# Kernel tuning notes

Measured on AMD Instinct MI355X. Metric: run time of the kernel, lower is better.

## Reference

```python
import jax, jax.numpy as jnp
import numpy as np

B, T, C, HD = 4, 4096, 1024, 64

def setup_inputs() -> dict:
    key = jax.random.key(0)
    k1, k2, k3, k4 = jax.random.split(key, 4)
    x = jax.random.normal(k1, (B, T, C), dtype=jnp.float32)
    scale = 1.0 / np.sqrt(C)
    Wq = jax.random.normal(k2, (C, HD), dtype=jnp.float32) * scale
    Wk = jax.random.normal(k3, (C, HD), dtype=jnp.float32) * scale
    Wv = jax.random.normal(k4, (C, HD), dtype=jnp.float32) * scale
    return {"x": x, "Wq": Wq, "Wk": Wk, "Wv": Wv}

def reference(x, Wq, Wk, Wv):
    # q,k,v: [B,T,HD]
    q = jnp.einsum('btc,ch->bth', x, Wq)
    k = jnp.einsum('btc,ch->bth', x, Wk)
    v = jnp.einsum('btc,ch->bth', x, Wv)
    hd = q.shape[-1]
    scores = jnp.einsum('bth,bsh->bts', q, k) / jnp.sqrt(jnp.float32(hd))  # [B,T,T]
    causal = jnp.tril(jnp.ones((scores.shape[1], scores.shape[1]), dtype=bool))
    scores = jnp.where(causal, scores, -jnp.inf)
    attn = jax.nn.softmax(scores, axis=-1)
    return jnp.einsum('bts,bsh->bth', attn, v)  # [B,T,HD]
```

## Files before the change

### kernel.cpp

```cpp
#include <hip/hip_runtime.h>
#include <hip/hip_bf16.h>

typedef __attribute__((ext_vector_type(8))) short bf16x8;
typedef __attribute__((ext_vector_type(4))) short bf16x4;
typedef __attribute__((ext_vector_type(4))) float f32x4;
typedef __attribute__((ext_vector_type(4))) int   i32x4;

#define C2LOG 0.18033688011112042f

__device__ __forceinline__ short f2bf(float f) {
    union { float f; unsigned u; } v; v.f = f;
    unsigned r = v.u + 0x7fff + ((v.u >> 16) & 1);
    return (short)(r >> 16);
}
__device__ __forceinline__ unsigned packbf(float a, float b) {
    return (unsigned)(unsigned short)f2bf(a) | ((unsigned)(unsigned short)f2bf(b) << 16);
}
__device__ __forceinline__ float bf2f(short s) {
    union { unsigned u; float f; } v; v.u = ((unsigned)(unsigned short)s) << 16;
    return v.f;
}

#define BB 4
#define TT 4096
#define CC 1024
#define HD 64
#define NTASK_PB 144
#define NTASK (BB * NTASK_PB)

__global__ void prep_w(const float* __restrict__ Wq, const float* __restrict__ Wk,
                       const float* __restrict__ Wv, short* __restrict__ Wt) {
    const int n = blockIdx.x;
    const float* W = (n < 64) ? Wq : (n < 128) ? Wk : Wv;
    const int col = n & 63;
    for (int k = threadIdx.x; k < CC; k += blockDim.x)
        Wt[n * CC + k] = f2bf(W[k * HD + col]);
}

__global__ __launch_bounds__(512) void proj_qkv(const float* __restrict__ x,
        const short* __restrict__ Wt, short* __restrict__ Q,
        short* __restrict__ K, short* __restrict__ Vt) {
    __shared__ short xs[2][32 * 72];
    __shared__ short wsm[2][192 * 64];

    const int tid  = threadIdx.x;
    const int lane = tid & 63;
    const int wv   = tid >> 6;
    const int lm   = lane & 15;
    const int lg   = lane >> 4;
    const int mhalf = wv & 1;
    const int ngrp  = wv >> 1;
    const int mbase = blockIdx.x * 32;

    const int xr  = tid >> 4;
    const int xq4 = tid & 15;
    const float* xrow = x + (size_t)(mbase + xr) * CC;

    int wsrow[3], wscol[3];
    #pragma unroll
    for (int it = 0; it < 3; ++it) {
        const int off = it * 8192 + wv * 1024 + lane * 16;
        wsrow[it] = off >> 7;
        wscol[it] = (off & 127) ^ ((wsrow[it] & 7) << 4);
    }

#define STAGE_W(bufidx, kc)                                                           \
    {                                                                                 \
        _Pragma("unroll")                                                             \
        for (int it = 0; it < 3; ++it) {                                              \
            const char* src = (const char*)(Wt + (size_t)wsrow[it] * CC + (kc) * 64)  \
                              + wscol[it];                                            \
            char* dst = (char*)&wsm[bufidx][0] + it * 8192 + wv * 1024;               \
            __builtin_amdgcn_global_load_lds(                                         \
                (const __attribute__((address_space(1))) unsigned*)src,               \
                (__attribute__((address_space(3))) unsigned*)dst, 16, 0, 0);          \
        }                                                                             \
    }

#define CONV_X(bufidx, xv)                                                            \
    {                                                                                 \
        bf16x4 bv;                                                                    \
        bv[0] = f2bf((xv).x); bv[1] = f2bf((xv).y);                                   \
        bv[2] = f2bf((xv).z); bv[3] = f2bf((xv).w);                                   \
        *reinterpret_cast<bf16x4*>(&xs[bufidx][xr * 72 + xq4 * 4]) = bv;              \
    }

    f32x4 acc[3];
    #pragma unroll
    for (int i = 0; i < 3; ++i) acc[i] = f32x4{0.f, 0.f, 0.f, 0.f};

    {
        float4 v = *reinterpret_cast<const float4*>(xrow + xq4 * 4);
        CONV_X(0, v)
        STAGE_W(0, 0)
    }
    asm volatile("s_waitcnt vmcnt(0)" ::: "memory");
    __syncthreads();

    const int arow = mhalf * 16 + lm;
    int buf = 0;
    for (int kc = 0; kc < 16; ++kc) {
        float4 nv;
        const bool more = (kc < 15);
        if (more) {
            nv = *reinterpret_cast<const float4*>(xrow + (kc + 1) * 64 + xq4 * 4);
            STAGE_W(buf ^ 1, kc + 1)
        }

        bf16x8 a0 = *reinterpret_cast<const bf16x8*>(&xs[buf][arow * 72 + lg * 8]);
        bf16x8 a1 = *reinterpret_cast<const bf16x8*>(&xs[buf][arow * 72 + 32 + lg * 8]);
        #pragma unroll
        for (int c = 0; c < 3; ++c) {
            const int brow = (ngrp * 3 + c) * 16 + lm;
            const int sw = (brow & 7) << 4;
            bf16x8 b0 = *reinterpret_cast<const bf16x8*>(
                (const char*)&wsm[buf][0] + brow * 128 + ((lg * 16) ^ sw));
            bf16x8 b1 = *reinterpret_cast<const bf16x8*>(
                (const char*)&wsm[buf][0] + brow * 128 + ((64 + lg * 16) ^ sw));
            acc[c] = __builtin_amdgcn_mfma_f32_16x16x32_bf16(a0, b0, acc[c], 0, 0, 0);
            acc[c] = __builtin_amdgcn_mfma_f32_16x16x32_bf16(a1, b1, acc[c], 0, 0, 0);
        }

        if (more) CONV_X(buf ^ 1, nv)
        asm volatile("s_waitcnt vmcnt(0)" ::: "memory");
        __syncthreads();
        buf ^= 1;
    }
#undef STAGE_W
#undef CONV_X

    const int mrow = mbase + mhalf * 16 + lg * 4;
    #pragma unroll
    for (int c = 0; c < 3; ++c) {
        const int cn = ngrp * 3 + c;
        if (cn < 4) {
            #pragma unroll
            for (int r = 0; r < 4; ++r)
                Q[(size_t)(mrow + r) * HD + cn * 16 + lm] = f2bf(acc[c][r]);
        } else if (cn < 8) {
            #pragma unroll
            for (int r = 0; r < 4; ++r)
                K[(size_t)(mrow + r) * HD + (cn - 4) * 16 + lm] = f2bf(acc[c][r]);
        } else {
            const int bb   = mbase >> 12;
            const int tloc = (mbase & 4095) + mhalf * 16 + lg * 4;
            bf16x4 v4;
            #pragma unroll
            for (int r = 0; r < 4; ++r) v4[r] = f2bf(acc[c][r]);
            *reinterpret_cast<bf16x4*>(
                Vt + (size_t)bb * (HD * TT) + (size_t)((cn - 8) * 16 + lm) * TT + tloc) = v4;
        }
    }
}

__global__ __launch_bounds__(512, 4) void attn(const short* __restrict__ Q,
        const short* __restrict__ K, const short* __restrict__ Vt,
        short* __restrict__ Opart, float* __restrict__ Mpart,
        float* __restrict__ Lpart) {
    __shared__ short ks[2][64 * 64];
    __shared__ short vs[2][64 * 64];

    const int tid  = threadIdx.x;
    const int lane = tid & 63;
    const int wv   = tid >> 6;
    const int lm   = lane & 15;
    const int lg   = lane >> 4;

    const int task = blockIdx.x;
    const int b  = task / NTASK_PB;
    int t_in = task - b * NTASK_PB;
    int g = 0;
    while (t_in >= 2 * (g + 1) * (g + 2)) ++g;
    const int idx = t_in - 2 * g * (g + 1);
    const int i   = 4 * g + idx / (g + 1);
    const int seg = idx % (g + 1);
    const int S   = g + 1;
    const int niter = 2 * i + 2;
    const int qbase = i * 128;

    const size_t qkb = (size_t)b * TT * HD;
    const size_t vtb = (size_t)b * HD * TT;
    const int qrow = qbase + wv * 16;
    const int tmax = (qrow + 15) >> 6;

    bf16x8 qf0 = *reinterpret_cast<const bf16x8*>(Q + qkb + (size_t)(qrow + lm) * HD + lg * 8);
    bf16x8 qf1 = *reinterpret_cast<const bf16x8*>(Q + qkb + (size_t)(qrow + lm) * HD + 32 + lg * 8);

    f32x4 o[4];
    #pragma unroll
    for (int c = 0; c < 4; ++c) o[c] = f32x4{0.f, 0.f, 0.f, 0.f};
    float mrun = -1e30f, lrun = 0.f;

    const int srcA = lm + ((lane & 16) << 1);
    const int srcB = srcA + 16;
    const bool hihalf = (lane & 32) != 0;

    const int lds_off = (wv << 10) + (lane << 4);
    const int srow    = lds_off >> 7;
    const int scolb   = (lds_off & 127) ^ ((srow & 7) << 4);

#define STAGE_KV(bufidx, tt)                                                          \
    {                                                                                 \
        const char* ksrc = (const char*)(K + qkb) + (tt) * 8192 + (srow << 7) + scolb;\
        char* kdst = (char*)&ks[bufidx][0] + (wv << 10);                              \
        __builtin_amdgcn_global_load_lds(                                             \
            (const __attribute__((address_space(1))) unsigned*)ksrc,                  \
            (__attribute__((address_space(3))) unsigned*)kdst, 16, 0, 0);             \
        const char* vsrc = (const char*)(Vt + vtb) + (size_t)srow * (TT * 2)          \
                           + (tt) * 128 + scolb;                                      \
        char* vdst = (char*)&vs[bufidx][0] + (wv << 10);                              \
        __builtin_amdgcn_global_load_lds(                                             \
            (const __attribute__((address_space(1))) unsigned*)vsrc,                  \
            (__attribute__((address_space(3))) unsigned*)vdst, 16, 0, 0);             \
    }

    STAGE_KV(0, seg)
    asm volatile("s_waitcnt vmcnt(0)" ::: "memory");
    __syncthreads();

    int buf = 0;
    for (int t = seg; t < niter; t += S) {
        const int tn = t + S;
        if (tn < niter) STAGE_KV(buf ^ 1, tn)

        if (t <= tmax) {
            const short* ksb = &ks[buf][0];
            const short* vsb = &vs[buf][0];
            const int kv = t * 64;

            f32x4 st[4];
            #pragma unroll
            for (int kt = 0; kt < 4; ++kt) {
                const int krow = kt * 16 + lm;
                const int sw = (krow & 7) << 4;
                bf16x8 k0 = *reinterpret_cast<const bf16x8*>(
                    (const char*)ksb + krow * 128 + ((lg * 16) ^ sw));
                bf16x8 k1 = *reinterpret_cast<const bf16x8*>(
                    (const char*)ksb + krow * 128 + ((64 + lg * 16) ^ sw));
                f32x4 a = f32x4{0.f, 0.f, 0.f, 0.f};
                a = __builtin_amdgcn_mfma_f32_16x16x32_bf16(k0, qf0, a, 0, 0, 0);
                a = __builtin_amdgcn_mfma_f32_16x16x32_bf16(k1, qf1, a, 0, 0, 0);
                st[kt] = a;
            }
            float s2[4][4];
            #pragma unroll
            for (int kt = 0; kt < 4; ++kt)
                #pragma unroll
                for (int r = 0; r < 4; ++r) s2[kt][r] = st[kt][r] * C2LOG;
            if (kv + 63 > qrow) {
                const int qg = qrow + lm;
                #pragma unroll
                for (int kt = 0; kt < 4; ++kt)
                    #pragma unroll
                    for (int r = 0; r < 4; ++r)
                        if (kv + kt * 16 + lg * 4 + r > qg) s2[kt][r] = -1e30f;
            }
            float mloc = s2[0][0];
            #pragma unroll
            for (int kt = 0; kt < 4; ++kt)
                #pragma unroll
                for (int r = 0; r < 4; ++r) mloc = fmaxf(mloc, s2[kt][r]);
            mloc = fmaxf(mloc, __shfl_xor(mloc, 16));
            mloc = fmaxf(mloc, __shfl_xor(mloc, 32));
            const float mnew = fmaxf(mrun, mloc);
            const float alpha = __builtin_amdgcn_exp2f(mrun - mnew);
            mrun = mnew;

            float p[4][4];
            float rs = 0.f;
            #pragma unroll
            for (int kt = 0; kt < 4; ++kt)
                #pragma unroll
                for (int r = 0; r < 4; ++r) {
                    p[kt][r] = __builtin_amdgcn_exp2f(s2[kt][r] - mnew);
                    rs += p[kt][r];
                }
            rs += __shfl_xor(rs, 16);
            rs += __shfl_xor(rs, 32);
            lrun = lrun * alpha + rs;

            unsigned u[4][2];
            #pragma unroll
            for (int kt = 0; kt < 4; ++kt) {
                u[kt][0] = packbf(p[kt][0], p[kt][1]);
                u[kt][1] = packbf(p[kt][2], p[kt][3]);
            }
            #pragma unroll
            for (int c = 0; c < 4; ++c)
                #pragma unroll
                for (int r = 0; r < 4; ++r) o[c][r] *= alpha;

            #pragma unroll
            for (int h = 0; h < 2; ++h) {
                const int b0 = __shfl((int)u[2 * h][0], srcA);
                const int c0 = __shfl((int)u[2 * h + 1][0], srcA);
                const int b1 = __shfl((int)u[2 * h][1], srcA);
                const int c1 = __shfl((int)u[2 * h + 1][1], srcA);
                const int b2 = __shfl((int)u[2 * h][0], srcB);
                const int c2 = __shfl((int)u[2 * h + 1][0], srcB);
                const int b3 = __shfl((int)u[2 * h][1], srcB);
                const int c3 = __shfl((int)u[2 * h + 1][1], srcB);
                union { i32x4 iv; bf16x8 v; } cv;
                cv.iv = i32x4{ hihalf ? c0 : b0, hihalf ? c1 : b1,
                               hihalf ? c2 : b2, hihalf ? c3 : b3 };
                #pragma unroll
                for (int c = 0; c < 4; ++c) {
                    const int vrow = c * 16 + lm;
                    const int sw = (vrow & 7) << 4;
                    bf16x8 va = *reinterpret_cast<const bf16x8*>(
                        (const char*)vsb + vrow * 128 + ((h * 64 + lg * 16) ^ sw));
                    o[c] = __builtin_amdgcn_mfma_f32_16x16x32_bf16(va, cv.v, o[c], 0, 0, 0);
                }
            }
        }

        asm volatile("s_waitcnt vmcnt(0)" ::: "memory");
        __syncthreads();
        buf ^= 1;
    }
#undef STAGE_KV

    short* Ob = Opart + (size_t)task * (128 * HD);
    #pragma unroll
    for (int c = 0; c < 4; ++c) {
        bf16x4 ov;
        #pragma unroll
        for (int r = 0; r < 4; ++r) ov[r] = f2bf(o[c][r]);
        *reinterpret_cast<bf16x4*>(&Ob[(wv * 16 + lm) * HD + c * 16 + lg * 4]) = ov;
    }
    if (lg == 0) {
        Mpart[task * 128 + wv * 16 + lm] = mrun;
        Lpart[task * 128 + wv * 16 + lm] = lrun;
    }
}

__global__ __launch_bounds__(256) void combine(const short* __restrict__ Opart,
        const float* __restrict__ Mpart, const float* __restrict__ Lpart,
        float* __restrict__ out) {
    const int b   = blockIdx.x >> 8;
    const int rem = blockIdx.x & 255;
    const int i   = rem >> 3;
    const int rr  = rem & 7;
    const int g = i >> 2;
    const int S = g + 1;
    const int task0 = b * NTASK_PB + 2 * g * (g + 1) + (i - 4 * g) * (g + 1);
    const int qbase = i * 128;

    const int tid = threadIdx.x;
    const int row = rr * 16 + (tid >> 4);
    const int cb  = (tid & 15) << 2;

    float mmax = -1e30f;
    float ms[8];
    for (int s = 0; s < S; ++s) {
        ms[s] = Mpart[(task0 + s) * 128 + row];
        mmax = fmaxf(mmax, ms[s]);
    }
    float lsum = 0.f;
    float a0 = 0.f, a1 = 0.f, a2 = 0.f, a3 = 0.f;
    for (int s = 0; s < S; ++s) {
        const float w = __builtin_amdgcn_exp2f(ms[s] - mmax);
        lsum += Lpart[(task0 + s) * 128 + row] * w;
        bf16x4 ov = *reinterpret_cast<const bf16x4*>(
            &Opart[((size_t)(task0 + s) * 128 + row) * HD + cb]);
        a0 += bf2f(ov[0]) * w;
        a1 += bf2f(ov[1]) * w;
        a2 += bf2f(ov[2]) * w;
        a3 += bf2f(ov[3]) * w;
    }
    const float inv = 1.0f / lsum;
    f32x4 res{ a0 * inv, a1 * inv, a2 * inv, a3 * inv };
    *reinterpret_cast<f32x4*>(
        &out[((size_t)b * TT + qbase + row) * HD + cb]) = res;
}

extern "C" void kernel_launch(void* const* d_in, const int* in_sizes, int n_in,
                              void* d_out, int out_size, void* d_ws, size_t ws_size,
                              hipStream_t stream) {
    const float* x  = (const float*)d_in[0];
    const float* Wq = (const float*)d_in[1];
    const float* Wk = (const float*)d_in[2];
    const float* Wv = (const float*)d_in[3];
    float* out = (float*)d_out;

    char* ws = (char*)d_ws;
    short* Wt    = (short*)(ws);
    short* Q     = (short*)(ws + 393216);
    short* K     = (short*)(ws + 2490368);
    short* Vt    = (short*)(ws + 4587520);
    short* Opart = (short*)(ws + 6684672);
    float* Mpart = (float*)(ws + 16121856);
    float* Lpart = (float*)(ws + 16416768);

    hipLaunchKernelGGL(prep_w,   dim3(192),   dim3(256), 0, stream, Wq, Wk, Wv, Wt);
    hipLaunchKernelGGL(proj_qkv, dim3(512),   dim3(512), 0, stream, x, Wt, Q, K, Vt);
    hipLaunchKernelGGL(attn,     dim3(NTASK), dim3(512), 0, stream, Q, K, Vt,
                       Opart, Mpart, Lpart);
    hipLaunchKernelGGL(combine,  dim3(1024),  dim3(256), 0, stream,
                       Opart, Mpart, Lpart, out);
}
```

Before: 68.34 us.

## Process 32 query rows per wave in attention to reuse K/V LDS fragments

The attention block drops from 8 to 4 waves, and each wave now handles two 16-row query tiles. Every K and V fragment read from LDS therefore feeds two MFMAs instead of one, halving LDS read traffic per FLOP. Each thread stages twice as many K/V chunks per tile. In exchange, register pressure roughly doubles (two accumulator sets and duplicated softmax state), the launch bound changes to 256 threads with min 3 blocks, and fewer waves are available to hide latency.

```diff
diff --git a/kernel.cpp b/kernel.cpp
--- a/kernel.cpp
+++ b/kernel.cpp
@@ -153,7 +153,7 @@
     }
 }
 
-__global__ __launch_bounds__(512, 4) void attn(const short* __restrict__ Q,
+__global__ __launch_bounds__(256, 3) void attn(const short* __restrict__ Q,
         const short* __restrict__ K, const short* __restrict__ Vt,
         short* __restrict__ Opart, float* __restrict__ Mpart,
         float* __restrict__ Lpart) {
@@ -176,42 +176,52 @@
     const int seg = idx % (g + 1);
     const int S   = g + 1;
     const int niter = 2 * i + 2;
-    const int qbase = i * 128;
 
     const size_t qkb = (size_t)b * TT * HD;
     const size_t vtb = (size_t)b * HD * TT;
-    const int qrow = qbase + wv * 16;
-    const int tmax = (qrow + 15) >> 6;
+    const int qrow = i * 128 + wv * 32;
+    const int tmax = (qrow + 31) >> 6;
 
     bf16x8 qf0 = *reinterpret_cast<const bf16x8*>(Q + qkb + (size_t)(qrow + lm) * HD + lg * 8);
     bf16x8 qf1 = *reinterpret_cast<const bf16x8*>(Q + qkb + (size_t)(qrow + lm) * HD + 32 + lg * 8);
-
-    f32x4 o[4];
-    #pragma unroll
-    for (int c = 0; c < 4; ++c) o[c] = f32x4{0.f, 0.f, 0.f, 0.f};
-    float mrun = -1e30f, lrun = 0.f;
+    bf16x8 qf2 = *reinterpret_cast<const bf16x8*>(Q + qkb + (size_t)(qrow + 16 + lm) * HD + lg * 8);
+    bf16x8 qf3 = *reinterpret_cast<const bf16x8*>(Q + qkb + (size_t)(qrow + 16 + lm) * HD + 32 + lg * 8);
+
+    f32x4 oA[4], oB[4];
+    #pragma unroll
+    for (int c = 0; c < 4; ++c) { oA[c] = f32x4{0.f,0.f,0.f,0.f}; oB[c] = f32x4{0.f,0.f,0.f,0.f}; }
+    float mrunA = -1e30f, lrunA = 0.f;
+    float mrunB = -1e30f, lrunB = 0.f;
 
     const int srcA = lm + ((lane & 16) << 1);
     const int srcB = srcA + 16;
     const bool hihalf = (lane & 32) != 0;
 
-    const int lds_off = (wv << 10) + (lane << 4);
-    const int srow    = lds_off >> 7;
-    const int scolb   = (lds_off & 127) ^ ((srow & 7) << 4);
+    int srow[2], scol[2];
+    #pragma unroll
+    for (int c = 0; c < 2; ++c) {
+        const int off = wv * 2048 + c * 1024 + lane * 16;
+        srow[c] = off >> 7;
+        scol[c] = (off & 127) ^ ((srow[c] & 7) << 4);
+    }
 
 #define STAGE_KV(bufidx, tt)                                                          \
     {                                                                                 \
-        const char* ksrc = (const char*)(K + qkb) + (tt) * 8192 + (srow << 7) + scolb;\
-        char* kdst = (char*)&ks[bufidx][0] + (wv << 10);                              \
-        __builtin_amdgcn_global_load_lds(                                             \
-            (const __attribute__((address_space(1))) unsigned*)ksrc,                  \
-            (__attribute__((address_space(3))) unsigned*)kdst, 16, 0, 0);             \
-        const char* vsrc = (const char*)(Vt + vtb) + (size_t)srow * (TT * 2)          \
-                           + (tt) * 128 + scolb;                                      \
-        char* vdst = (char*)&vs[bufidx][0] + (wv << 10);                              \
-        __builtin_amdgcn_global_load_lds(                                             \
-            (const __attribute__((address_space(1))) unsigned*)vsrc,                  \
-            (__attribute__((address_space(3))) unsigned*)vdst, 16, 0, 0);             \
+        _Pragma("unroll")                                                             \
+        for (int c = 0; c < 2; ++c) {                                                 \
+            const char* ksrc = (const char*)(K + qkb) + (tt) * 8192                   \
+                               + (srow[c] << 7) + scol[c];                            \
+            char* kdst = (char*)&ks[bufidx][0] + wv * 2048 + c * 1024;                \
+            __builtin_amdgcn_global_load_lds(                                         \
+                (const __attribute__((address_space(1))) unsigned*)ksrc,              \
+                (__attribute__((address_space(3))) unsigned*)kdst, 16, 0, 0);         \
+            const char* vsrc = (const char*)(Vt + vtb) + (size_t)srow[c] * (TT * 2)   \
+                               + (tt) * 128 + scol[c];                                \
+            char* vdst = (char*)&vs[bufidx][0] + wv * 2048 + c * 1024;                \
+            __builtin_amdgcn_global_load_lds(                                         \
+                (const __attribute__((address_space(1))) unsigned*)vsrc,              \
+                (__attribute__((address_space(3))) unsigned*)vdst, 16, 0, 0);         \
+        }                                                                             \
     }
 
     STAGE_KV(0, seg)
@@ -228,7 +238,7 @@
             const short* vsb = &vs[buf][0];
             const int kv = t * 64;
 
-            f32x4 st[4];
+            f32x4 stA[4], stB[4];
             #pragma unroll
             for (int kt = 0; kt < 4; ++kt) {
                 const int krow = kt * 16 + lm;
@@ -237,79 +247,119 @@
                     (const char*)ksb + krow * 128 + ((lg * 16) ^ sw));
                 bf16x8 k1 = *reinterpret_cast<const bf16x8*>(
                     (const char*)ksb + krow * 128 + ((64 + lg * 16) ^ sw));
-                f32x4 a = f32x4{0.f, 0.f, 0.f, 0.f};
+                f32x4 a = f32x4{0.f,0.f,0.f,0.f};
                 a = __builtin_amdgcn_mfma_f32_16x16x32_bf16(k0, qf0, a, 0, 0, 0);
                 a = __builtin_amdgcn_mfma_f32_16x16x32_bf16(k1, qf1, a, 0, 0, 0);
-                st[kt] = a;
+                stA[kt] = a;
+                f32x4 bb2 = f32x4{0.f,0.f,0.f,0.f};
+                bb2 = __builtin_amdgcn_mfma_f32_16x16x32_bf16(k0, qf2, bb2, 0, 0, 0);
+                bb2 = __builtin_amdgcn_mfma_f32_16x16x32_bf16(k1, qf3, bb2, 0, 0, 0);
+                stB[kt] = bb2;
             }
-            float s2[4][4];
+
+            float s2A[4][4], s2B[4][4];
             #pragma unroll
             for (int kt = 0; kt < 4; ++kt)
                 #pragma unroll
-                for (int r = 0; r < 4; ++r) s2[kt][r] = st[kt][r] * C2LOG;
+                for (int r = 0; r < 4; ++r) {
+                    s2A[kt][r] = stA[kt][r] * C2LOG;
+                    s2B[kt][r] = stB[kt][r] * C2LOG;
+                }
             if (kv + 63 > qrow) {
-                const int qg = qrow + lm;
+                const int qgA = qrow + lm;
+                const int qgB = qrow + 16 + lm;
                 #pragma unroll
                 for (int kt = 0; kt < 4; ++kt)
                     #pragma unroll
-                    for (int r = 0; r < 4; ++r)
-                        if (kv + kt * 16 + lg * 4 + r > qg) s2[kt][r] = -1e30f;
+                    for (int r = 0; r < 4; ++r) {
+                        const int kk = kv + kt * 16 + lg * 4 + r;
+                        if (kk > qgA) s2A[kt][r] = -1e30f;
+                        if (kk > qgB) s2B[kt][r] = -1e30f;
+                    }
             }
-            float mloc = s2[0][0];
+
+            float mlocA = s2A[0][0], mlocB = s2B[0][0];
             #pragma unroll
             for (int kt = 0; kt < 4; ++kt)
                 #pragma unroll
-                for (int r = 0; r < 4; ++r) mloc = fmaxf(mloc, s2[kt][r]);
-            mloc = fmaxf(mloc, __shfl_xor(mloc, 16));
-            mloc = fmaxf(mloc, __shfl_xor(mloc, 32));
-            const float mnew = fmaxf(mrun, mloc);
-            const float alpha = __builtin_amdgcn_exp2f(mrun - mnew);
-            mrun = mnew;
-
-            float p[4][4];
-            float rs = 0.f;
+                for (int r = 0; r < 4; ++r) {
+                    mlocA = fmaxf(mlocA, s2A[kt][r]);
+                    mlocB = fmaxf(mlocB, s2B[kt][r]);
+                }
+            mlocA = fmaxf(mlocA, __shfl_xor(mlocA, 16));
+            mlocA = fmaxf(mlocA, __shfl_xor(mlocA, 32));
+            mlocB = fmaxf(mlocB, __shfl_xor(mlocB, 16));
+            mlocB = fmaxf(mlocB, __shfl_xor(mlocB, 32));
+            const float mnewA = fmaxf(mrunA, mlocA);
+            const float mnewB = fmaxf(mrunB, mlocB);
+            const float alphaA = __builtin_amdgcn_exp2f(mrunA - mnewA);
+            const float alphaB = __builtin_amdgcn_exp2f(mrunB - mnewB);
+            mrunA = mnewA; mrunB = mnewB;
+
+            float pA[4][4], pB[4][4];
+            float rsA = 0.f, rsB = 0.f;
             #pragma unroll
             for (int kt = 0; kt < 4; ++kt)
                 #pragma unroll
                 for (int r = 0; r < 4; ++r) {
-                    p[kt][r] = __builtin_amdgcn_exp2f(s2[kt][r] - mnew);
-                    rs += p[kt][r];
+                    pA[kt][r] = __builtin_amdgcn_exp2f(s2A[kt][r] - mnewA);
+                    rsA += pA[kt][r];
+                    pB[kt][r] = __builtin_amdgcn_exp2f(s2B[kt][r] - mnewB);
+                    rsB += pB[kt][r];
                 }
-            rs += __shfl_xor(rs, 16);
-            rs += __shfl_xor(rs, 32);
-            lrun = lrun * alpha + rs;
-
-            unsigned u[4][2];
+            rsA += __shfl_xor(rsA, 16); rsA += __shfl_xor(rsA, 32);
+            rsB += __shfl_xor(rsB, 16); rsB += __shfl_xor(rsB, 32);
+            lrunA = lrunA * alphaA + rsA;
+            lrunB = lrunB * alphaB + rsB;
+
+            unsigned uA[4][2], uB[4][2];
             #pragma unroll
             for (int kt = 0; kt < 4; ++kt) {
-                u[kt][0] = packbf(p[kt][0], p[kt][1]);
-                u[kt][1] = packbf(p[kt][2], p[kt][3]);
+                uA[kt][0] = packbf(pA[kt][0], pA[kt][1]);
+                uA[kt][1] = packbf(pA[kt][2], pA[kt][3]);
+                uB[kt][0] = packbf(pB[kt][0], pB[kt][1]);
+                uB[kt][1] = packbf(pB[kt][2], pB[kt][3]);
             }
             #pragma unroll
             for (int c = 0; c < 4; ++c)
                 #pragma unroll
-                for (int r = 0; r < 4; ++r) o[c][r] *= alpha;
+                for (int r = 0; r < 4; ++r) {
+                    oA[c][r] *= alphaA;
+                    oB[c][r] *= alphaB;
+                }
 
             #pragma unroll
             for (int h = 0; h < 2; ++h) {
-                const int b0 = __shfl((int)u[2 * h][0], srcA);
-                const int c0 = __shfl((int)u[2 * h + 1][0], srcA);
-                const int b1 = __shfl((int)u[2 * h][1], srcA);
-                const int c1 = __shfl((int)u[2 * h + 1][1], srcA);
-                const int b2 = __shfl((int)u[2 * h][0], srcB);
-                const int c2 = __shfl((int)u[2 * h + 1][0], srcB);
-                const int b3 = __shfl((int)u[2 * h][1], srcB);
-                const int c3 = __shfl((int)u[2 * h + 1][1], srcB);
-                union { i32x4 iv; bf16x8 v; } cv;
-                cv.iv = i32x4{ hihalf ? c0 : b0, hihalf ? c1 : b1,
-                               hihalf ? c2 : b2, hihalf ? c3 : b3 };
+                const int a0 = __shfl((int)uA[2*h][0],   srcA);
+                const int a1c = __shfl((int)uA[2*h+1][0], srcA);
+                const int a2 = __shfl((int)uA[2*h][1],   srcA);
+                const int a3c = __shfl((int)uA[2*h+1][1], srcA);
+                const int a4 = __shfl((int)uA[2*h][0],   srcB);
+                const int a5c = __shfl((int)uA[2*h+1][0], srcB);
+                const int a6 = __shfl((int)uA[2*h][1],   srcB);
+                const int a7c = __shfl((int)uA[2*h+1][1], srcB);
+                union { i32x4 iv; bf16x8 v; } cvA;
+                cvA.iv = i32x4{ hihalf ? a1c : a0, hihalf ? a3c : a2,
+                                hihalf ? a5c : a4, hihalf ? a7c : a6 };
+                const int b0 = __shfl((int)uB[2*h][0],   srcA);
+                const int b1c = __shfl((int)uB[2*h+1][0], srcA);
+                const int b2 = __shfl((int)uB[2*h][1],   srcA);
+                const int b3c = __shfl((int)uB[2*h+1][1], srcA);
+                const int b4 = __shfl((int)uB[2*h][0],   srcB);
+                const int b5c = __shfl((int)uB[2*h+1][0], srcB);
+                const int b6 = __shfl((int)uB[2*h][1],   srcB);
+                const int b7c = __shfl((int)uB[2*h+1][1], srcB);
+                union { i32x4 iv; bf16x8 v; } cvB;
+                cvB.iv = i32x4{ hihalf ? b1c : b0, hihalf ? b3c : b2,
+                                hihalf ? b5c : b4, hihalf ? b7c : b6 };
                 #pragma unroll
                 for (int c = 0; c < 4; ++c) {
                     const int vrow = c * 16 + lm;
                     const int sw = (vrow & 7) << 4;
                     bf16x8 va = *reinterpret_cast<const bf16x8*>(
                         (const char*)vsb + vrow * 128 + ((h * 64 + lg * 16) ^ sw));
-                    o[c] = __builtin_amdgcn_mfma_f32_16x16x32_bf16(va, cv.v, o[c], 0, 0, 0);
+                    oA[c] = __builtin_amdgcn_mfma_f32_16x16x32_bf16(va, cvA.v, oA[c], 0, 0, 0);
+                    oB[c] = __builtin_amdgcn_mfma_f32_16x16x32_bf16(va, cvB.v, oB[c], 0, 0, 0);
                 }
             }
         }
@@ -323,14 +373,17 @@
     short* Ob = Opart + (size_t)task * (128 * HD);
     #pragma unroll
     for (int c = 0; c < 4; ++c) {
-        bf16x4 ov;
+        bf16x4 ovA, ovB;
         #pragma unroll
-        for (int r = 0; r < 4; ++r) ov[r] = f2bf(o[c][r]);
-        *reinterpret_cast<bf16x4*>(&Ob[(wv * 16 + lm) * HD + c * 16 + lg * 4]) = ov;
+        for (int r = 0; r < 4; ++r) { ovA[r] = f2bf(oA[c][r]); ovB[r] = f2bf(oB[c][r]); }
+        *reinterpret_cast<bf16x4*>(&Ob[(wv * 32 + lm) * HD + c * 16 + lg * 4]) = ovA;
+        *reinterpret_cast<bf16x4*>(&Ob[(wv * 32 + 16 + lm) * HD + c * 16 + lg * 4]) = ovB;
     }
     if (lg == 0) {
-        Mpart[task * 128 + wv * 16 + lm] = mrun;
-        Lpart[task * 128 + wv * 16 + lm] = lrun;
+        Mpart[task * 128 + wv * 32 + lm] = mrunA;
+        Lpart[task * 128 + wv * 32 + lm] = lrunA;
+        Mpart[task * 128 + wv * 32 + 16 + lm] = mrunB;
+        Lpart[task * 128 + wv * 32 + 16 + lm] = lrunB;
     }
 }
 
@@ -394,7 +447,7 @@
 
     hipLaunchKernelGGL(prep_w,   dim3(192),   dim3(256), 0, stream, Wq, Wk, Wv, Wt);
     hipLaunchKernelGGL(proj_qkv, dim3(512),   dim3(512), 0, stream, x, Wt, Q, K, Vt);
-    hipLaunchKernelGGL(attn,     dim3(NTASK), dim3(512), 0, stream, Q, K, Vt,
+    hipLaunchKernelGGL(attn,     dim3(NTASK), dim3(256), 0, stream, Q, K, Vt,
                        Opart, Mpart, Lpart);
     hipLaunchKernelGGL(combine,  dim3(1024),  dim3(256), 0, stream,
                        Opart, Mpart, Lpart, out);
```

After: 69.52 us. No clear change (+1.7%).
